# Performance work log

Measured on AMD Instinct MI355X. Metric: run time of the kernel, lower is better.

## Reference

```python
import jax, jax.numpy as jnp
import numpy as np

NUM_GRAPHS = 512  # number of segments (graphs) in the batch


def setup_inputs() -> dict:
    key = jax.random.key(0)
    k1, k2, k3, k4, k5, k6 = jax.random.split(key, 6)
    N, Din, D, H = 100000, 1024, 64, 32
    x = jax.random.normal(k1, (N, Din), dtype=jnp.float32)
    batch = jnp.sort(jax.random.randint(k2, (N,), 0, NUM_GRAPHS)).astype(jnp.int64)
    W_enc = jax.random.normal(k3, (D, Din), dtype=jnp.float32) * (1.0 / np.sqrt(Din))
    b_enc = jax.random.normal(k4, (D,), dtype=jnp.float32) * 0.01
    W_gate = jax.random.normal(k5, (H, D), dtype=jnp.float32) * (1.0 / np.sqrt(D))
    b_gate = jax.random.normal(k6, (H,), dtype=jnp.float32) * 0.01
    return {"x": x, "batch": batch, "W_enc": W_enc, "b_enc": b_enc,
            "W_gate": W_gate, "b_gate": b_gate}


def reference(x, batch, W_enc, b_enc, W_gate, b_gate):
    B = NUM_GRAPHS
    batch = batch.astype(jnp.int32)
    # shared encoder: [N, Din] -> [N, D]
    xe = jnp.dot(x, W_enc.T) + b_enc
    # all 32 heads' scalar gates at once: [N, H]
    gate = jnp.dot(xe, W_gate.T) + b_gate
    # segment-wise (per-graph) stable softmax over nodes, per head
    gmax = jax.ops.segment_max(gate, batch, num_segments=B)          # [B, H]
    g = jnp.exp(gate - gmax[batch])                                   # [N, H]
    gsum = jax.ops.segment_sum(g, batch, num_segments=B)             # [B, H]
    alpha = g / gsum[batch]                                           # [N, H]
    # scatter-weighted sum: out[b,h,d] = sum_{n in graph b} alpha[n,h]*xe[n,d]
    weighted = alpha[:, :, None] * xe[:, None, :]                     # [N, H, D]
    pooled = jax.ops.segment_sum(weighted, batch, num_segments=B)    # [B, H, D]
    # concat over heads (head i occupies cols [i*D, (i+1)*D)) then ReLU
    return jax.nn.relu(pooled.reshape(B, -1))
```

## Files before the change

### kernel.cpp

```cpp
#include <hip/hip_runtime.h>


typedef short bf16x8 __attribute__((ext_vector_type(8)));
typedef float f32x4 __attribute__((ext_vector_type(4)));

#define NUM_GRAPHS 512
#define DIN 1024
#define DENC 64
#define NH 32
#define LDA 72
#define LDB 72

__device__ __forceinline__ unsigned short f2bf(float f) {
    unsigned int u = __float_as_uint(f);
    return (unsigned short)((u + 0x7fffu + ((u >> 16) & 1u)) >> 16);
}
__device__ __forceinline__ void split2(float f, unsigned short& h, unsigned short& l) {
    unsigned int u = __float_as_uint(f);
    unsigned int hb = (u + 0x7fffu + ((u >> 16) & 1u)) >> 16;
    h = (unsigned short)hb;
    float hf = __uint_as_float(hb << 16);
    l = f2bf(f - hf);
}

__device__ __forceinline__ int clampseg(int v) {
    return v < 0 ? 0 : (v >= NUM_GRAPHS ? NUM_GRAPHS - 1 : v);
}

__global__ void k_seg(const int* __restrict__ batch, int* __restrict__ seg, int N) {
    int n = blockIdx.x * 256 + threadIdx.x;
    if (n >= N) return;
    int bc = clampseg(batch[n]);
    if (n == 0) {
        for (int j = 0; j <= bc; ++j) seg[j] = 0;
        int bl = clampseg(batch[N - 1]);
        for (int j = bl + 1; j <= NUM_GRAPHS; ++j) seg[j] = N;
    } else {
        int bp = clampseg(batch[n - 1]);
        for (int j = bp + 1; j <= bc; ++j) seg[j] = n;
    }
}

__global__ void k_convw(const float* __restrict__ W,
                        unsigned short* __restrict__ Wh,
                        unsigned short* __restrict__ Wl) {
    int idx = (blockIdx.x * 256 + threadIdx.x) * 4;
    float4 v = *(const float4*)(W + idx);
    ushort4 h4, l4;
    split2(v.x, h4.x, l4.x);
    split2(v.y, h4.y, l4.y);
    split2(v.z, h4.z, l4.z);
    split2(v.w, h4.w, l4.w);
    *(ushort4*)(Wh + idx) = h4;
    *(ushort4*)(Wl + idx) = l4;
}

__global__ __launch_bounds__(256, 2) void k_gemm(
    const float* __restrict__ x,
    const unsigned short* __restrict__ Wh,
    const unsigned short* __restrict__ Wl,
    const float* __restrict__ b_enc,
    float* __restrict__ xe,
    int N)
{
    __shared__ unsigned short Ah[128 * LDA], Al[128 * LDA];
    __shared__ unsigned short Bh[64 * LDB],  Bl[64 * LDB];

    const int tid  = threadIdx.x;
    const int lane = tid & 63;
    const int wv   = tid >> 6;
    const long brow = (long)blockIdx.x * 128;

    f32x4 acc[2][4];
    #pragma unroll
    for (int i = 0; i < 2; ++i)
        #pragma unroll
        for (int j = 0; j < 4; ++j) acc[i][j] = (f32x4){0.f, 0.f, 0.f, 0.f};

    const int ar0 = tid >> 4;
    const int ac4 = (tid & 15) * 4;
    const int br0 = tid >> 3;
    const int bc8 = (tid & 7) * 8;
    const int fr  = lane & 15;
    const int fq  = lane >> 4;

    for (int k0 = 0; k0 < DIN; k0 += 64) {
        #pragma unroll
        for (int i = 0; i < 8; ++i) {
            int row = ar0 + 16 * i;
            long gr = brow + row;
            float4 v = {0.f, 0.f, 0.f, 0.f};
            if (gr < N) v = *(const float4*)(x + gr * DIN + k0 + ac4);
            ushort4 h4, l4;
            split2(v.x, h4.x, l4.x);
            split2(v.y, h4.y, l4.y);
            split2(v.z, h4.z, l4.z);
            split2(v.w, h4.w, l4.w);
            *(ushort4*)&Ah[row * LDA + ac4] = h4;
            *(ushort4*)&Al[row * LDA + ac4] = l4;
        }
        #pragma unroll
        for (int i = 0; i < 2; ++i) {
            int row = br0 + 32 * i;
            *(uint4*)&Bh[row * LDB + bc8] = *(const uint4*)(Wh + row * DIN + k0 + bc8);
            *(uint4*)&Bl[row * LDB + bc8] = *(const uint4*)(Wl + row * DIN + k0 + bc8);
        }
        __syncthreads();

        #pragma unroll
        for (int kk = 0; kk < 64; kk += 32) {
            bf16x8 ah[2], al[2];
            #pragma unroll
            for (int rt = 0; rt < 2; ++rt) {
                int o = (wv * 32 + rt * 16 + fr) * LDA + fq * 8 + kk;
                ah[rt] = *(const bf16x8*)&Ah[o];
                al[rt] = *(const bf16x8*)&Al[o];
            }
            #pragma unroll
            for (int ct = 0; ct < 4; ++ct) {
                int o = (ct * 16 + fr) * LDB + fq * 8 + kk;
                bf16x8 bh = *(const bf16x8*)&Bh[o];
                bf16x8 bl = *(const bf16x8*)&Bl[o];
                #pragma unroll
                for (int rt = 0; rt < 2; ++rt) {
                    acc[rt][ct] = __builtin_amdgcn_mfma_f32_16x16x32_bf16(ah[rt], bh, acc[rt][ct], 0, 0, 0);
                    acc[rt][ct] = __builtin_amdgcn_mfma_f32_16x16x32_bf16(ah[rt], bl, acc[rt][ct], 0, 0, 0);
                    acc[rt][ct] = __builtin_amdgcn_mfma_f32_16x16x32_bf16(al[rt], bh, acc[rt][ct], 0, 0, 0);
                }
            }
        }
        __syncthreads();
    }

    float bv[4];
    #pragma unroll
    for (int ct = 0; ct < 4; ++ct) bv[ct] = b_enc[ct * 16 + fr];
    #pragma unroll
    for (int rt = 0; rt < 2; ++rt) {
        #pragma unroll
        for (int r = 0; r < 4; ++r) {
            long row = brow + wv * 32 + rt * 16 + fq * 4 + r;
            if (row < N) {
                float* o = xe + row * DENC;
                #pragma unroll
                for (int ct = 0; ct < 4; ++ct)
                    o[ct * 16 + fr] = acc[rt][ct][r] + bv[ct];
            }
        }
    }
}

__global__ __launch_bounds__(256) void k_gate(
    const float* __restrict__ xe,
    const float* __restrict__ Wg,
    const float* __restrict__ bg,
    float* __restrict__ gate,
    int N)
{
    __shared__ float xs[128 * 68];
    __shared__ float wgs[32 * 68];
    __shared__ float bgs[32];
    const int tid = threadIdx.x;
    const long brow = (long)blockIdx.x * 128;

    for (int i = tid; i < NH * DENC; i += 256) wgs[(i >> 6) * 68 + (i & 63)] = Wg[i];
    if (tid < NH) bgs[tid] = bg[tid];

    const int r0s = tid >> 4, c4 = (tid & 15) * 4;
    #pragma unroll
    for (int i = 0; i < 8; ++i) {
        int row = r0s + 16 * i;
        long gr = brow + row;
        if (gr < N)
            *(float4*)&xs[row * 68 + c4] = *(const float4*)(xe + gr * DENC + c4);
    }
    __syncthreads();

    const int r0 = tid & 31;
    const int h0 = (tid >> 5) * 4;
    float acc[4][4] = {};
    #pragma unroll
    for (int k = 0; k < 64; k += 4) {
        float4 w0 = *(const float4*)&wgs[(h0 + 0) * 68 + k];
        float4 w1 = *(const float4*)&wgs[(h0 + 1) * 68 + k];
        float4 w2 = *(const float4*)&wgs[(h0 + 2) * 68 + k];
        float4 w3 = *(const float4*)&wgs[(h0 + 3) * 68 + k];
        #pragma unroll
        for (int i = 0; i < 4; ++i) {
            float4 xv = *(const float4*)&xs[(r0 + 32 * i) * 68 + k];
            acc[i][0] += xv.x * w0.x + xv.y * w0.y + xv.z * w0.z + xv.w * w0.w;
            acc[i][1] += xv.x * w1.x + xv.y * w1.y + xv.z * w1.z + xv.w * w1.w;
            acc[i][2] += xv.x * w2.x + xv.y * w2.y + xv.z * w2.z + xv.w * w2.w;
            acc[i][3] += xv.x * w3.x + xv.y * w3.y + xv.z * w3.z + xv.w * w3.w;
        }
    }
    #pragma unroll
    for (int i = 0; i < 4; ++i) {
        long row = brow + r0 + 32 * i;
        if (row < N) {
            float4 o = { acc[i][0] + bgs[h0 + 0], acc[i][1] + bgs[h0 + 1],
                         acc[i][2] + bgs[h0 + 2], acc[i][3] + bgs[h0 + 3] };
            *(float4*)(gate + row * NH + h0) = o;
        }
    }
}

__global__ __launch_bounds__(256) void k_pool(
    const float* __restrict__ xe,
    const float* __restrict__ gate,
    const int* __restrict__ seg,
    float* __restrict__ out,
    int N)
{
    __shared__ float xs[64 * 68];
    __shared__ float gs[64 * 36];
    __shared__ float gmaxs[NH];
    __shared__ float gsums[NH];
    const int tid = threadIdx.x;
    const int b = blockIdx.x;
    const int s = seg[b], e = seg[b + 1];
    const long ob = (long)b * (NH * DENC);
    if (e <= s) {
        for (int i = tid; i < NH * DENC; i += 256) out[ob + i] = 0.f;
        return;
    }
    const int rl = tid & 63;
    const int hq = tid >> 6;
    const int h0 = hq * 8;

    float vmax[8];
    #pragma unroll
    for (int j = 0; j < 8; ++j) vmax[j] = -INFINITY;
    for (int base = s; base < e; base += 64) {
        if (base + rl < e) {
            const float* g0 = gate + (long)(base + rl) * NH + h0;
            float4 a = *(const float4*)g0;
            float4 c = *(const float4*)(g0 + 4);
            vmax[0] = fmaxf(vmax[0], a.x); vmax[1] = fmaxf(vmax[1], a.y);
            vmax[2] = fmaxf(vmax[2], a.z); vmax[3] = fmaxf(vmax[3], a.w);
            vmax[4] = fmaxf(vmax[4], c.x); vmax[5] = fmaxf(vmax[5], c.y);
            vmax[6] = fmaxf(vmax[6], c.z); vmax[7] = fmaxf(vmax[7], c.w);
        }
    }
    #pragma unroll
    for (int off = 32; off > 0; off >>= 1)
        #pragma unroll
        for (int j = 0; j < 8; ++j) vmax[j] = fmaxf(vmax[j], __shfl_down(vmax[j], off));
    if (rl == 0)
        #pragma unroll
        for (int j = 0; j < 8; ++j) gmaxs[h0 + j] = vmax[j];
    __syncthreads();
    float gm[8];
    #pragma unroll
    for (int j = 0; j < 8; ++j) gm[j] = gmaxs[h0 + j];

    float pool[8] = {0, 0, 0, 0, 0, 0, 0, 0};
    float gp[8] = {0, 0, 0, 0, 0, 0, 0, 0};
    const int r0s = tid >> 4, c4 = (tid & 15) * 4;
    for (int base = s; base < e; base += 64) {
        const int nrow = min(64, e - base);
        #pragma unroll
        for (int i = 0; i < 4; ++i) {
            int row = r0s + 16 * i;
            if (row < nrow)
                *(float4*)&xs[row * 68 + c4] = *(const float4*)(xe + (long)(base + row) * DENC + c4);
        }
        float4 ga = {0, 0, 0, 0}, gb = {0, 0, 0, 0};
        if (rl < nrow) {
            const float* g0 = gate + (long)(base + rl) * NH + h0;
            float4 a = *(const float4*)g0;
            float4 c = *(const float4*)(g0 + 4);
            ga.x = __expf(a.x - gm[0]); ga.y = __expf(a.y - gm[1]);
            ga.z = __expf(a.z - gm[2]); ga.w = __expf(a.w - gm[3]);
            gb.x = __expf(c.x - gm[4]); gb.y = __expf(c.y - gm[5]);
            gb.z = __expf(c.z - gm[6]); gb.w = __expf(c.w - gm[7]);
            gp[0] += ga.x; gp[1] += ga.y; gp[2] += ga.z; gp[3] += ga.w;
            gp[4] += gb.x; gp[5] += gb.y; gp[6] += gb.z; gp[7] += gb.w;
        }
        *(float4*)&gs[rl * 36 + h0] = ga;
        *(float4*)&gs[rl * 36 + h0 + 4] = gb;
        __syncthreads();
        #pragma unroll 4
        for (int r2 = 0; r2 < nrow; ++r2) {
            float xv = xs[r2 * 68 + rl];
            float4 g1 = *(const float4*)&gs[r2 * 36 + h0];
            float4 g2 = *(const float4*)&gs[r2 * 36 + h0 + 4];
            pool[0] += g1.x * xv; pool[1] += g1.y * xv;
            pool[2] += g1.z * xv; pool[3] += g1.w * xv;
            pool[4] += g2.x * xv; pool[5] += g2.y * xv;
            pool[6] += g2.z * xv; pool[7] += g2.w * xv;
        }
        __syncthreads();
    }
    #pragma unroll
    for (int off = 32; off > 0; off >>= 1)
        #pragma unroll
        for (int j = 0; j < 8; ++j) gp[j] += __shfl_down(gp[j], off);
    if (rl == 0)
        #pragma unroll
        for (int j = 0; j < 8; ++j) gsums[h0 + j] = gp[j];
    __syncthreads();
    #pragma unroll
    for (int j = 0; j < 8; ++j) {
        float v = pool[j] / gsums[h0 + j];
        out[ob + (h0 + j) * DENC + rl] = fmaxf(v, 0.f);
    }
}

extern "C" void kernel_launch(void* const* d_in, const int* in_sizes, int n_in,
                              void* d_out, int out_size, void* d_ws, size_t ws_size,
                              hipStream_t stream)
{
    const float* x      = (const float*)d_in[0];
    const int* batch    = (const int*)d_in[1];
    const float* W_enc  = (const float*)d_in[2];
    const float* b_enc  = (const float*)d_in[3];
    const float* W_gate = (const float*)d_in[4];
    const float* b_gate = (const float*)d_in[5];
    float* out = (float*)d_out;
    const int N = in_sizes[1];

    char* ws = (char*)d_ws;
    size_t off = 0;
    auto take = [&](size_t bytes) {
        char* p = ws + off;
        off += (bytes + 255) & ~(size_t)255;
        return p;
    };
    float* xe  = (float*)take((size_t)N * DENC * sizeof(float));
    float* gate = (float*)take((size_t)N * NH * sizeof(float));
    unsigned short* Wh = (unsigned short*)take((size_t)DENC * DIN * 2);
    unsigned short* Wl = (unsigned short*)take((size_t)DENC * DIN * 2);
    int* seg = (int*)take((NUM_GRAPHS + 1) * sizeof(int));
    (void)ws_size; (void)n_in; (void)out_size;

    k_seg<<<(N + 255) / 256, 256, 0, stream>>>(batch, seg, N);
    k_convw<<<(DENC * DIN) / 1024, 256, 0, stream>>>(W_enc, Wh, Wl);
    k_gemm<<<(N + 127) / 128, 256, 0, stream>>>(x, Wh, Wl, b_enc, xe, N);
    k_gate<<<(N + 127) / 128, 256, 0, stream>>>(xe, W_gate, b_gate, gate, N);
    k_pool<<<NUM_GRAPHS, 256, 0, stream>>>(xe, gate, seg, out, N);
}
```

Measured before the change: 710.4 us.

## Prefetch GEMM tiles into registers, fuse prep kernels, use online softmax in pooling

Register-prefetches the next K-slice of x and the split weights in the encoder GEMM while the current slice is being multiplied, so global load latency overlaps with MFMA work. Merges the segment-boundary and weight-split kernels into one launch. Replaces the pooling kernel's separate max pass over gates with an online-softmax rescaling, which removes one read of the gate array. In exchange the GEMM holds more registers, which may lower occupancy, and the pooling loop does more exp and shuffle work per chunk.

```diff
diff --git a/kernel.cpp b/kernel.cpp
--- a/kernel.cpp
+++ b/kernel.cpp
@@ -27,32 +27,36 @@
     return v < 0 ? 0 : (v >= NUM_GRAPHS ? NUM_GRAPHS - 1 : v);
 }
 
-__global__ void k_seg(const int* __restrict__ batch, int* __restrict__ seg, int N) {
-    int n = blockIdx.x * 256 + threadIdx.x;
-    if (n >= N) return;
-    int bc = clampseg(batch[n]);
-    if (n == 0) {
-        for (int j = 0; j <= bc; ++j) seg[j] = 0;
-        int bl = clampseg(batch[N - 1]);
-        for (int j = bl + 1; j <= NUM_GRAPHS; ++j) seg[j] = N;
+__global__ void k_prep(const int* __restrict__ batch, int* __restrict__ seg, int N,
+                       const float* __restrict__ W,
+                       unsigned short* __restrict__ Wh,
+                       unsigned short* __restrict__ Wl,
+                       int nseg_blocks)
+{
+    const int blk = blockIdx.x;
+    if (blk < nseg_blocks) {
+        int n = blk * 256 + threadIdx.x;
+        if (n >= N) return;
+        int bc = clampseg(batch[n]);
+        if (n == 0) {
+            for (int j = 0; j <= bc; ++j) seg[j] = 0;
+            int bl = clampseg(batch[N - 1]);
+            for (int j = bl + 1; j <= NUM_GRAPHS; ++j) seg[j] = N;
+        } else {
+            int bp = clampseg(batch[n - 1]);
+            for (int j = bp + 1; j <= bc; ++j) seg[j] = n;
+        }
     } else {
-        int bp = clampseg(batch[n - 1]);
-        for (int j = bp + 1; j <= bc; ++j) seg[j] = n;
-    }
-}
-
-__global__ void k_convw(const float* __restrict__ W,
-                        unsigned short* __restrict__ Wh,
-                        unsigned short* __restrict__ Wl) {
-    int idx = (blockIdx.x * 256 + threadIdx.x) * 4;
-    float4 v = *(const float4*)(W + idx);
-    ushort4 h4, l4;
-    split2(v.x, h4.x, l4.x);
-    split2(v.y, h4.y, l4.y);
-    split2(v.z, h4.z, l4.z);
-    split2(v.w, h4.w, l4.w);
-    *(ushort4*)(Wh + idx) = h4;
-    *(ushort4*)(Wl + idx) = l4;
+        int idx = ((blk - nseg_blocks) * 256 + threadIdx.x) * 4;
+        float4 v = *(const float4*)(W + idx);
+        ushort4 h4, l4;
+        split2(v.x, h4.x, l4.x);
+        split2(v.y, h4.y, l4.y);
+        split2(v.z, h4.z, l4.z);
+        split2(v.w, h4.w, l4.w);
+        *(ushort4*)(Wh + idx) = h4;
+        *(ushort4*)(Wl + idx) = l4;
+    }
 }
 
 __global__ __launch_bounds__(256, 2) void k_gemm(
@@ -84,28 +88,59 @@
     const int fr  = lane & 15;
     const int fq  = lane >> 4;
 
+    float4 va[8];
+    uint4  vbh[2], vbl[2];
+
+    #pragma unroll
+    for (int i = 0; i < 8; ++i) {
+        int row = ar0 + 16 * i;
+        long gr = brow + row;
+        va[i] = (gr < N) ? *(const float4*)(x + gr * DIN + ac4)
+                         : (float4){0.f, 0.f, 0.f, 0.f};
+    }
+    #pragma unroll
+    for (int i = 0; i < 2; ++i) {
+        int row = br0 + 32 * i;
+        vbh[i] = *(const uint4*)(Wh + row * DIN + bc8);
+        vbl[i] = *(const uint4*)(Wl + row * DIN + bc8);
+    }
+
     for (int k0 = 0; k0 < DIN; k0 += 64) {
         #pragma unroll
         for (int i = 0; i < 8; ++i) {
             int row = ar0 + 16 * i;
-            long gr = brow + row;
-            float4 v = {0.f, 0.f, 0.f, 0.f};
-            if (gr < N) v = *(const float4*)(x + gr * DIN + k0 + ac4);
             ushort4 h4, l4;
-            split2(v.x, h4.x, l4.x);
-            split2(v.y, h4.y, l4.y);
-            split2(v.z, h4.z, l4.z);
-            split2(v.w, h4.w, l4.w);
+            split2(va[i].x, h4.x, l4.x);
+            split2(va[i].y, h4.y, l4.y);
+            split2(va[i].z, h4.z, l4.z);
+            split2(va[i].w, h4.w, l4.w);
             *(ushort4*)&Ah[row * LDA + ac4] = h4;
             *(ushort4*)&Al[row * LDA + ac4] = l4;
         }
         #pragma unroll
         for (int i = 0; i < 2; ++i) {
             int row = br0 + 32 * i;
-            *(uint4*)&Bh[row * LDB + bc8] = *(const uint4*)(Wh + row * DIN + k0 + bc8);
-            *(uint4*)&Bl[row * LDB + bc8] = *(const uint4*)(Wl + row * DIN + k0 + bc8);
+            *(uint4*)&Bh[row * LDB + bc8] = vbh[i];
+            *(uint4*)&Bl[row * LDB + bc8] = vbl[i];
         }
         __syncthreads();
+
+        const int kn = k0 + 64;
+        if (kn < DIN) {
+            #pragma unroll
+            for (int i = 0; i < 8; ++i) {
+                int row = ar0 + 16 * i;
+                long gr = brow + row;
+                va[i] = (gr < N) ? *(const float4*)(x + gr * DIN + kn + ac4)
+                                 : (float4){0.f, 0.f, 0.f, 0.f};
+            }
+            #pragma unroll
+            for (int i = 0; i < 2; ++i) {
+                int row = br0 + 32 * i;
+                vbh[i] = *(const uint4*)(Wh + row * DIN + kn + bc8);
+                vbl[i] = *(const uint4*)(Wl + row * DIN + kn + bc8);
+            }
+        }
 
         #pragma unroll
         for (int kk = 0; kk < 64; kk += 32) {
@@ -214,8 +249,6 @@
 {
     __shared__ float xs[64 * 68];
     __shared__ float gs[64 * 36];
-    __shared__ float gmaxs[NH];
-    __shared__ float gsums[NH];
     const int tid = threadIdx.x;
     const int b = blockIdx.x;
     const int s = seg[b], e = seg[b + 1];
@@ -227,36 +260,12 @@
     const int rl = tid & 63;
     const int hq = tid >> 6;
     const int h0 = hq * 8;
-
-    float vmax[8];
-    #pragma unroll
-    for (int j = 0; j < 8; ++j) vmax[j] = -INFINITY;
-    for (int base = s; base < e; base += 64) {
-        if (base + rl < e) {
-            const float* g0 = gate + (long)(base + rl) * NH + h0;
-            float4 a = *(const float4*)g0;
-            float4 c = *(const float4*)(g0 + 4);
-            vmax[0] = fmaxf(vmax[0], a.x); vmax[1] = fmaxf(vmax[1], a.y);
-            vmax[2] = fmaxf(vmax[2], a.z); vmax[3] = fmaxf(vmax[3], a.w);
-            vmax[4] = fmaxf(vmax[4], c.x); vmax[5] = fmaxf(vmax[5], c.y);
-            vmax[6] = fmaxf(vmax[6], c.z); vmax[7] = fmaxf(vmax[7], c.w);
-        }
-    }
-    #pragma unroll
-    for (int off = 32; off > 0; off >>= 1)
-        #pragma unroll
-        for (int j = 0; j < 8; ++j) vmax[j] = fmaxf(vmax[j], __shfl_down(vmax[j], off));
-    if (rl == 0)
-        #pragma unroll
-        for (int j = 0; j < 8; ++j) gmaxs[h0 + j] = vmax[j];
-    __syncthreads();
-    float gm[8];
-    #pragma unroll
-    for (int j = 0; j < 8; ++j) gm[j] = gmaxs[h0 + j];
-
-    float pool[8] = {0, 0, 0, 0, 0, 0, 0, 0};
-    float gp[8] = {0, 0, 0, 0, 0, 0, 0, 0};
     const int r0s = tid >> 4, c4 = (tid & 15) * 4;
+
+    float m[8], pool[8], gp[8];
+    #pragma unroll
+    for (int j = 0; j < 8; ++j) { m[j] = -INFINITY; pool[j] = 0.f; gp[j] = 0.f; }
+
     for (int base = s; base < e; base += 64) {
         const int nrow = min(64, e - base);
         #pragma unroll
@@ -265,15 +274,40 @@
             if (row < nrow)
                 *(float4*)&xs[row * 68 + c4] = *(const float4*)(xe + (long)(base + row) * DENC + c4);
         }
-        float4 ga = {0, 0, 0, 0}, gb = {0, 0, 0, 0};
-        if (rl < nrow) {
+        float gv[8];
+        const bool valid = (rl < nrow);
+        if (valid) {
             const float* g0 = gate + (long)(base + rl) * NH + h0;
             float4 a = *(const float4*)g0;
             float4 c = *(const float4*)(g0 + 4);
-            ga.x = __expf(a.x - gm[0]); ga.y = __expf(a.y - gm[1]);
-            ga.z = __expf(a.z - gm[2]); ga.w = __expf(a.w - gm[3]);
-            gb.x = __expf(c.x - gm[4]); gb.y = __expf(c.y - gm[5]);
-            gb.z = __expf(c.z - gm[6]); gb.w = __expf(c.w - gm[7]);
+            gv[0] = a.x; gv[1] = a.y; gv[2] = a.z; gv[3] = a.w;
+            gv[4] = c.x; gv[5] = c.y; gv[6] = c.z; gv[7] = c.w;
+        } else {
+            #pragma unroll
+            for (int j = 0; j < 8; ++j) gv[j] = -INFINITY;
+        }
+        float cm[8];
+        #pragma unroll
+        for (int j = 0; j < 8; ++j) cm[j] = gv[j];
+        #pragma unroll
+        for (int off = 32; off > 0; off >>= 1)
+            #pragma unroll
+            for (int j = 0; j < 8; ++j) cm[j] = fmaxf(cm[j], __shfl_xor(cm[j], off));
+        #pragma unroll
+        for (int j = 0; j < 8; ++j) {
+            if (cm[j] > m[j]) {
+                float sc = (m[j] == -INFINITY) ? 0.f : __expf(m[j] - cm[j]);
+                pool[j] *= sc;
+                gp[j]   *= sc;
+                m[j] = cm[j];
+            }
+        }
+        float4 ga = {0.f, 0.f, 0.f, 0.f}, gb = {0.f, 0.f, 0.f, 0.f};
+        if (valid) {
+            ga.x = __expf(gv[0] - m[0]); ga.y = __expf(gv[1] - m[1]);
+            ga.z = __expf(gv[2] - m[2]); ga.w = __expf(gv[3] - m[3]);
+            gb.x = __expf(gv[4] - m[4]); gb.y = __expf(gv[5] - m[5]);
+            gb.z = __expf(gv[6] - m[6]); gb.w = __expf(gv[7] - m[7]);
             gp[0] += ga.x; gp[1] += ga.y; gp[2] += ga.z; gp[3] += ga.w;
             gp[4] += gb.x; gp[5] += gb.y; gp[6] += gb.z; gp[7] += gb.w;
         }
@@ -295,14 +329,10 @@
     #pragma unroll
     for (int off = 32; off > 0; off >>= 1)
         #pragma unroll
-        for (int j = 0; j < 8; ++j) gp[j] += __shfl_down(gp[j], off);
-    if (rl == 0)
-        #pragma unroll
-        for (int j = 0; j < 8; ++j) gsums[h0 + j] = gp[j];
-    __syncthreads();
+        for (int j = 0; j < 8; ++j) gp[j] += __shfl_xor(gp[j], off);
     #pragma unroll
     for (int j = 0; j < 8; ++j) {
-        float v = pool[j] / gsums[h0 + j];
+        float v = pool[j] / gp[j];
         out[ob + (h0 + j) * DENC + rl] = fmaxf(v, 0.f);
     }
 }
@@ -334,8 +364,9 @@
     int* seg = (int*)take((NUM_GRAPHS + 1) * sizeof(int));
     (void)ws_size; (void)n_in; (void)out_size;
 
-    k_seg<<<(N + 255) / 256, 256, 0, stream>>>(batch, seg, N);
-    k_convw<<<(DENC * DIN) / 1024, 256, 0, stream>>>(W_enc, Wh, Wl);
+    const int nseg_blocks = (N + 255) / 256;
+    const int nconv_blocks = (DENC * DIN) / 1024;
+    k_prep<<<nseg_blocks + nconv_blocks, 256, 0, stream>>>(batch, seg, N, W_enc, Wh, Wl, nseg_blocks);
     k_gemm<<<(N + 127) / 128, 256, 0, stream>>>(x, Wh, Wl, b_enc, xe, N);
     k_gate<<<(N + 127) / 128, 256, 0, stream>>>(xe, W_gate, b_gate, gate, N);
     k_pool<<<NUM_GRAPHS, 256, 0, stream>>>(xe, gate, seg, out, N);
```

Result: faster. 643.3 us (-9.4%).
